# Kernel tuning notes

Measured on AMD Instinct MI355X. Metric: run time of the kernel, lower is better.

## Reference

```python
import jax, jax.numpy as jnp
import numpy as np

NUM_HEADS = 16

def _alibi(S, H, dtype):
    # fairseq-style ALiBi: slopes[h] * -(|i-j|), H assumed power of 2
    start = 2.0 ** (-8.0 / H)
    slopes = start ** jnp.arange(1, H + 1, dtype=jnp.float32)      # [H]
    pos = jnp.arange(S)
    rel = -jnp.abs(pos[None, :] - pos[:, None]).astype(jnp.float32)  # [S,S]
    return (slopes[:, None, None] * rel).astype(dtype)             # [H,S,S]

def setup_inputs() -> dict:
    key = jax.random.key(0)
    kx, km, kw1, kw2 = jax.random.split(key, 4)
    B, S, D = 2, 2048, 1024
    inputs = jax.random.normal(kx, (B, S, D), dtype=jnp.float32)
    mask = jax.random.bernoulli(km, 0.9, (B, S))
    mask = mask.at[:, 0].set(True)  # ensure each row has a valid key
    Wqkv = jax.random.normal(kw1, (3 * D, D), dtype=jnp.float32) * 0.02
    bqkv = jnp.zeros((3 * D,), dtype=jnp.float32)
    Wproj = jax.random.normal(kw2, (D, D), dtype=jnp.float32) * 0.02
    bproj = jnp.zeros((D,), dtype=jnp.float32)
    return {"inputs": inputs, "mask": mask, "Wqkv": Wqkv, "bqkv": bqkv,
            "Wproj": Wproj, "bproj": bproj}

def reference(inputs, mask, Wqkv, bqkv, Wproj, bproj):
    B, S, D = inputs.shape
    H = NUM_HEADS
    dh = D // H
    scale = D ** (-0.5)  # NOTE: original scales by full dim, not head dim
    qkv = inputs @ Wqkv.T + bqkv                       # [B,S,3D]
    qkv = qkv.reshape(B, S, H, 3 * dh).transpose(0, 2, 1, 3)  # [B,H,S,3dh]
    q, k, v = qkv[..., :dh], qkv[..., dh:2 * dh], qkv[..., 2 * dh:]
    attn = jnp.einsum('bhqd,bhkd->bhqk', q, k) * scale  # [B,H,S,S]
    attn = attn + _alibi(S, H, attn.dtype)[None]
    attn = jnp.where(mask[:, None, None, :], attn, jnp.finfo(attn.dtype).min)
    attn = jax.nn.softmax(attn, axis=-1)
    x = jnp.einsum('bhqk,bhkd->bhqd', attn, v)          # [B,H,S,dh]
    x = x.transpose(0, 2, 1, 3).reshape(B, S, D)
    return x @ Wproj.T + bproj
```

## Files before the change

kernel.cpp:

```cpp
#include <hip/hip_runtime.h>
#include <cstdint>
#include <cstddef>

#define B_  2
#define S_  2048
#define D_  1024
#define H_  16
#define DH_ 64
#define M_  (B_*S_)
#define N3_ (3*D_)
#define NT_ (S_/64)

typedef float f32x4 __attribute__((ext_vector_type(4)));
typedef short short8 __attribute__((ext_vector_type(8)));
typedef unsigned short u16x8 __attribute__((ext_vector_type(8)));
typedef unsigned short u16x4 __attribute__((ext_vector_type(4)));

__device__ __forceinline__ unsigned short f2bf(float x) {
    unsigned int u = __float_as_uint(x);
    unsigned int r = (u + 0x7FFFu + ((u >> 16) & 1u)) >> 16;
    return (unsigned short)r;
}

__device__ __forceinline__ float exp2_(float x) { return __builtin_amdgcn_exp2f(x); }

__device__ __forceinline__ unsigned int cvt_pk_bf16(float a, float b) {
    unsigned int r;
    asm volatile("v_cvt_pk_bf16_f32 %0, %1, %2" : "=v"(r) : "v"(a), "v"(b));
    return r;
}

__device__ __forceinline__ void gload16(const void* g, void* l) {
    __builtin_amdgcn_global_load_lds(
        (const __attribute__((address_space(1))) unsigned int*)g,
        (__attribute__((address_space(3))) unsigned int*)l,
        16, 0, 0);
}

__global__ void k_detect_mask(const unsigned char* __restrict__ mb, int* __restrict__ flag) {
    __shared__ int sBig, sM4, sM8;
    if (threadIdx.x == 0) { sBig = 0; sM4 = 0; sM8 = 0; }
    __syncthreads();
    int big = 0, m4 = 0, m8 = 0;
    for (int i = threadIdx.x; i < 4096; i += blockDim.x) {
        unsigned char v = mb[i];
        if (v > 1) big = 1;
        if (v && (i & 3)) m4 = 1;
        if (v && ((i & 7) == 4)) m8 = 1;
    }
    if (big) atomicOr(&sBig, 1);
    if (m4)  atomicOr(&sM4, 1);
    if (m8)  atomicOr(&sM8, 1);
    __syncthreads();
    if (threadIdx.x == 0) {
        int w;
        if (sBig)      w = 0;
        else if (sM4)  w = 1;
        else if (sM8)  w = 4;
        else           w = 8;
        *flag = w;
    }
}

__global__ void k_maskbits(const void* __restrict__ mask, const int* __restrict__ flag,
                           unsigned long long* __restrict__ bits) {
    int i = blockIdx.x * 64 + threadIdx.x;
    int w = *flag;
    bool on;
    if (w == 0)      on = ((const float*)mask)[i] != 0.0f;
    else if (w == 1) on = ((const unsigned char*)mask)[i] != 0;
    else if (w == 4) on = ((const int*)mask)[i] != 0;
    else             on = ((const long long*)mask)[i] != 0;
    unsigned long long bal = __ballot(on);
    if (threadIdx.x == 0) bits[blockIdx.x] = bal;
}

__global__ void k_f2bf(const float* __restrict__ in, unsigned short* __restrict__ out, int n) {
    int i = (blockIdx.x * blockDim.x + threadIdx.x) * 4;
    if (i >= n) return;
    float4 v = *reinterpret_cast<const float4*>(&in[i]);
    u16x4 o = { f2bf(v.x), f2bf(v.y), f2bf(v.z), f2bf(v.w) };
    *reinterpret_cast<u16x4*>(&out[i]) = o;
}

template <bool OUT_BF16>
__global__ __launch_bounds__(256) void k_gemm_bf16_nt(
    const unsigned short* __restrict__ A, const unsigned short* __restrict__ W,
    const float* __restrict__ bias, void* __restrict__ Cout,
    int M, int N, int K) {
    __shared__ __align__(16) unsigned short Al[128 * 64];
    __shared__ __align__(16) unsigned short Wl[128 * 64];

    const int tid  = threadIdx.x;
    const int lane = tid & 63;
    const int w    = tid >> 6;
    const int wr   = w >> 1, wc = w & 1;
    const int l16  = lane & 15, g = lane >> 4;
    const int m0 = blockIdx.y * 128, n0 = blockIdx.x * 128;

    f32x4 acc[4][4];
#pragma unroll
    for (int m = 0; m < 4; ++m)
#pragma unroll
        for (int n = 0; n < 4; ++n) acc[m][n] = (f32x4){0.f, 0.f, 0.f, 0.f};

    const int srow = tid >> 3, scol = (tid & 7) * 8;

    for (int k0 = 0; k0 < K; k0 += 64) {
        __syncthreads();
#pragma unroll
        for (int i = 0; i < 4; ++i) {
            const int c = i * 256 + tid;
            const int row = srow + i * 32;
            gload16(A + (size_t)(m0 + row) * K + k0 + scol, Al + c * 8);
            gload16(W + (size_t)(n0 + row) * K + k0 + scol, Wl + c * 8);
        }
        __syncthreads();

#pragma unroll
        for (int kk = 0; kk < 2; ++kk) {
            short8 a[4], b[4];
#pragma unroll
            for (int m = 0; m < 4; ++m)
                a[m] = *reinterpret_cast<const short8*>(
                    &Al[(size_t)(wr * 64 + m * 16 + l16) * 64 + kk * 32 + g * 8]);
#pragma unroll
            for (int n = 0; n < 4; ++n)
                b[n] = *reinterpret_cast<const short8*>(
                    &Wl[(size_t)(wc * 64 + n * 16 + l16) * 64 + kk * 32 + g * 8]);
#pragma unroll
            for (int m = 0; m < 4; ++m)
#pragma unroll
                for (int n = 0; n < 4; ++n)
                    acc[m][n] = __builtin_amdgcn_mfma_f32_16x16x32_bf16(a[m], b[n], acc[m][n], 0, 0, 0);
        }
    }

    float bv[4];
#pragma unroll
    for (int n = 0; n < 4; ++n) bv[n] = bias[n0 + wc * 64 + n * 16 + l16];
#pragma unroll
    for (int m = 0; m < 4; ++m) {
#pragma unroll
        for (int r = 0; r < 4; ++r) {
            const size_t row = m0 + wr * 64 + m * 16 + g * 4 + r;
#pragma unroll
            for (int n = 0; n < 4; ++n) {
                const int col = n0 + wc * 64 + n * 16 + l16;
                float v = acc[m][n][r] + bv[n];
                if (OUT_BF16)
                    ((unsigned short*)Cout)[row * N + col] = f2bf(v);
                else
                    ((float*)Cout)[row * N + col] = v;
            }
        }
    }
}

__global__ __launch_bounds__(256) void k_attn_mfma(
    const unsigned short* __restrict__ qkv,
    const unsigned long long* __restrict__ mbits,
    unsigned short* __restrict__ x) {
    __shared__ __align__(16) unsigned short Kt[64][72];
    __shared__ __align__(16) unsigned short Vt[64][72];
    __shared__ __align__(16) unsigned short QP[64][72];

    const int tid  = threadIdx.x;
    const int lane = tid & 63;
    const int wq   = tid >> 6;
    const int g    = lane >> 4;
    const int g4   = g * 4;
    const int l16  = lane & 15;

    const int nqt = S_ / 64;
    const int qt = blockIdx.x % nqt;
    const int h  = (blockIdx.x / nqt) % H_;
    const int b  = blockIdx.x / (nqt * H_);
    const int q0 = qt * 64;
    const size_t rowbase = (size_t)b * S_ * N3_;
    const int hq = h * 192, hk = hq + 64, hv = hq + 128;
    const unsigned short* kvb = qkv + rowbase;

    {
        const int row = tid >> 2, cb = (tid & 3) * 16;
        const unsigned short* src = kvb + (size_t)(q0 + row) * N3_ + hq + cb;
        *reinterpret_cast<u16x8*>(&QP[row][cb])     = *reinterpret_cast<const u16x8*>(src);
        *reinterpret_cast<u16x8*>(&QP[row][cb + 8]) = *reinterpret_cast<const u16x8*>(src + 8);
    }
    __syncthreads();

    const short8 qa0 = *reinterpret_cast<const short8*>(&QP[wq*16 + l16][g*8]);
    const short8 qa1 = *reinterpret_cast<const short8*>(&QP[wq*16 + l16][32 + g*8]);

    f32x4 Oacc[4];
#pragma unroll
    for (int df = 0; df < 4; ++df) Oacc[df] = (f32x4){0.f, 0.f, 0.f, 0.f};
    float m = -1e30f, l = 0.0f;

    const float LOG2E = 1.4426950408889634f;
    const float c1 = 0.03125f * LOG2E;
    const float c2 = exp2f(-0.5f * (float)(h + 1)) * LOG2E;
    const int   qg = q0 + wq * 16 + l16;
    float albr[4];
#pragma unroll
    for (int r = 0; r < 4; ++r) albr[r] = c2 * (float)(g4 + r);
    const float c2_16 = c2 * 16.0f;

    const int krow = tid >> 2, kcb = (tid & 3) * 16;
    const int vkb = (tid & 15) * 4, vdb = (tid >> 4) * 4;
    u16x8 kr0, kr1;
    u16x4 vr0, vr1, vr2, vr3;

    {
        const unsigned short* ks = kvb + (size_t)krow * N3_ + hk + kcb;
        kr0 = *reinterpret_cast<const u16x8*>(ks);
        kr1 = *reinterpret_cast<const u16x8*>(ks + 8);
        const unsigned short* vs = kvb + (size_t)vkb * N3_ + hv + vdb;
        vr0 = *reinterpret_cast<const u16x4*>(vs);
        vr1 = *reinterpret_cast<const u16x4*>(vs + N3_);
        vr2 = *reinterpret_cast<const u16x4*>(vs + 2 * N3_);
        vr3 = *reinterpret_cast<const u16x4*>(vs + 3 * N3_);
    }

    for (int t = 0; t < NT_; ++t) {
        const int k0 = t * 64;
        __syncthreads();

        *reinterpret_cast<u16x8*>(&Kt[krow][kcb])     = kr0;
        *reinterpret_cast<u16x8*>(&Kt[krow][kcb + 8]) = kr1;
        {
            u16x4 w0 = { vr0.x, vr1.x, vr2.x, vr3.x };
            u16x4 w1 = { vr0.y, vr1.y, vr2.y, vr3.y };
            u16x4 w2 = { vr0.z, vr1.z, vr2.z, vr3.z };
            u16x4 w3 = { vr0.w, vr1.w, vr2.w, vr3.w };
            *reinterpret_cast<u16x4*>(&Vt[vdb + 0][vkb]) = w0;
            *reinterpret_cast<u16x4*>(&Vt[vdb + 1][vkb]) = w1;
            *reinterpret_cast<u16x4*>(&Vt[vdb + 2][vkb]) = w2;
            *reinterpret_cast<u16x4*>(&Vt[vdb + 3][vkb]) = w3;
        }
        if (t + 1 < NT_) {
            const int kn = k0 + 64;
            const unsigned short* ks = kvb + (size_t)(kn + krow) * N3_ + hk + kcb;
            kr0 = *reinterpret_cast<const u16x8*>(ks);
            kr1 = *reinterpret_cast<const u16x8*>(ks + 8);
            const unsigned short* vs = kvb + (size_t)(kn + vkb) * N3_ + hv + vdb;
            vr0 = *reinterpret_cast<const u16x4*>(vs);
            vr1 = *reinterpret_cast<const u16x4*>(vs + N3_);
            vr2 = *reinterpret_cast<const u16x4*>(vs + 2 * N3_);
            vr3 = *reinterpret_cast<const u16x4*>(vs + 3 * N3_);
        }
        __syncthreads();

        float p_[4][4];
#pragma unroll
        for (int jb = 0; jb < 4; ++jb) {
            short8 kb0 = *reinterpret_cast<const short8*>(&Kt[jb*16 + l16][g*8]);
            short8 kb1 = *reinterpret_cast<const short8*>(&Kt[jb*16 + l16][32 + g*8]);
            f32x4 c = (f32x4){0.f, 0.f, 0.f, 0.f};
            c = __builtin_amdgcn_mfma_f32_16x16x32_bf16(kb0, qa0, c, 0, 0, 0);
            c = __builtin_amdgcn_mfma_f32_16x16x32_bf16(kb1, qa1, c, 0, 0, 0);
#pragma unroll
            for (int r = 0; r < 4; ++r) p_[jb][r] = c[r];
        }

        if (k0 < q0) {
            const float tb = c2 * (float)(k0 - qg);
#pragma unroll
            for (int jb = 0; jb < 4; ++jb) {
                const float tbj = tb + c2_16 * (float)jb;
#pragma unroll
                for (int r = 0; r < 4; ++r)
                    p_[jb][r] = fmaf(p_[jb][r], c1, tbj + albr[r]);
            }
        } else if (k0 > q0) {
            const float tb = c2 * (float)(k0 - qg);
#pragma unroll
            for (int jb = 0; jb < 4; ++jb) {
                const float tbj = -tb - c2_16 * (float)jb;
#pragma unroll
                for (int r = 0; r < 4; ++r)
                    p_[jb][r] = fmaf(p_[jb][r], c1, tbj - albr[r]);
            }
        } else {
            const int dbase = k0 - qg;
#pragma unroll
            for (int jb = 0; jb < 4; ++jb)
#pragma unroll
                for (int r = 0; r < 4; ++r) {
                    int d = dbase + jb * 16 + g4 + r;
                    d = d < 0 ? -d : d;
                    p_[jb][r] = fmaf(p_[jb][r], c1, -c2 * (float)d);
                }
        }

        float mx = p_[0][0];
#pragma unroll
        for (int jb = 0; jb < 4; ++jb)
#pragma unroll
            for (int r = 0; r < 4; ++r) mx = fmaxf(mx, p_[jb][r]);
        mx = fmaxf(mx, __shfl_xor(mx, 16));
        mx = fmaxf(mx, __shfl_xor(mx, 32));

        if (__any(mx > m + 8.0f)) {
            const float mn = fmaxf(m, mx);
            const float cr = exp2_(m - mn);
            m = mn;
            l *= cr;
            const int srcb = (lane & 48) + ((lane & 48) >> 2);
#pragma unroll
            for (int r = 0; r < 4; ++r) {
                const float crq = __shfl(cr, srcb + r);
#pragma unroll
                for (int df = 0; df < 4; ++df) Oacc[df][r] *= crq;
            }
        }

        const unsigned long long mb = mbits[b * NT_ + t];
        const unsigned long long msh = mb >> g4;
        const unsigned int mw0 = (unsigned int)msh;
        const unsigned int mw1 = (unsigned int)(msh >> 32);
        float ps = 0.0f;
#pragma unroll
        for (int jb = 0; jb < 4; ++jb)
#pragma unroll
            for (int r = 0; r < 4; ++r) {
                float p = exp2_(p_[jb][r] - m);
                const unsigned int w = (jb < 2) ? mw0 : mw1;
                const int idx = (jb & 1) * 16 + r;
                p = ((w >> idx) & 1u) ? p : 0.0f;
                p_[jb][r] = p;
                ps += p;
            }
        ps += __shfl_xor(ps, 16);
        ps += __shfl_xor(ps, 32);
        l += ps;

#pragma unroll
        for (int jb = 0; jb < 4; ++jb) {
            uint2 st;
            st.x = cvt_pk_bf16(p_[jb][0], p_[jb][1]);
            st.y = cvt_pk_bf16(p_[jb][2], p_[jb][3]);
            *reinterpret_cast<uint2*>(&QP[wq*16 + l16][jb*16 + g4]) = st;
        }

        const short8 pa0 = *reinterpret_cast<const short8*>(&QP[wq*16 + l16][g*8]);
        const short8 pa1 = *reinterpret_cast<const short8*>(&QP[wq*16 + l16][32 + g*8]);
#pragma unroll
        for (int df = 0; df < 4; ++df) {
            short8 vb0 = *reinterpret_cast<const short8*>(&Vt[df*16 + l16][g*8]);
            short8 vb1 = *reinterpret_cast<const short8*>(&Vt[df*16 + l16][32 + g*8]);
            Oacc[df] = __builtin_amdgcn_mfma_f32_16x16x32_bf16(pa0, vb0, Oacc[df], 0, 0, 0);
            Oacc[df] = __builtin_amdgcn_mfma_f32_16x16x32_bf16(pa1, vb1, Oacc[df], 0, 0, 0);
        }
    }

    const int srcb = (lane & 48) + ((lane & 48) >> 2);
    float invq[4];
#pragma unroll
    for (int r = 0; r < 4; ++r) invq[r] = 1.0f / __shfl(l, srcb + r);
#pragma unroll
    for (int df = 0; df < 4; ++df) {
#pragma unroll
        for (int r = 0; r < 4; ++r) {
            const int qrow = q0 + wq * 16 + g4 + r;
            x[(size_t)(b * S_ + qrow) * D_ + h * 64 + df * 16 + l16] = f2bf(Oacc[df][r] * invq[r]);
        }
    }
}

extern "C" void kernel_launch(void* const* d_in, const int* in_sizes, int n_in,
                              void* d_out, int out_size, void* d_ws, size_t ws_size,
                              hipStream_t stream) {
    const float* inputs = (const float*)d_in[0];
    const void*  mask   = d_in[1];
    const float* Wqkv   = (const float*)d_in[2];
    const float* bqkv   = (const float*)d_in[3];
    const float* Wproj  = (const float*)d_in[4];
    const float* bproj  = (const float*)d_in[5];
    float* out = (float*)d_out;

    unsigned short* qkvb = (unsigned short*)d_ws;
    unsigned short* xb   = qkvb + (size_t)M_ * N3_;
    unsigned short* Ab   = xb + (size_t)M_ * D_;
    unsigned short* Wqb  = Ab + (size_t)M_ * D_;
    unsigned short* Wpb  = Wqb + (size_t)N3_ * D_;
    unsigned long long* bits = (unsigned long long*)(Wpb + (size_t)D_ * D_);
    int* flag = (int*)(bits + B_ * NT_);

    k_detect_mask<<<1, 256, 0, stream>>>((const unsigned char*)mask, flag);
    k_maskbits<<<B_ * NT_, 64, 0, stream>>>(mask, flag, bits);

    k_f2bf<<<(M_ * D_ / 4 + 255) / 256, 256, 0, stream>>>(inputs, Ab, M_ * D_);
    k_f2bf<<<(N3_ * D_ / 4 + 255) / 256, 256, 0, stream>>>(Wqkv, Wqb, N3_ * D_);
    k_f2bf<<<(D_ * D_ / 4 + 255) / 256, 256, 0, stream>>>(Wproj, Wpb, D_ * D_);

    dim3 g1(N3_ / 128, M_ / 128);
    k_gemm_bf16_nt<true><<<g1, 256, 0, stream>>>(Ab, Wqb, bqkv, qkvb, M_, N3_, D_);

    k_attn_mfma<<<B_ * H_ * (S_ / 64), 256, 0, stream>>>(qkvb, bits, xb);

    dim3 g2(D_ / 128, M_ / 128);
    k_gemm_bf16_nt<false><<<g2, 256, 0, stream>>>(xb, Wpb, bproj, out, M_, D_, D_);
}
```

Baseline: 194.2 us.

## Precompute additive mask in LDS, add MFMA priority hints, defer row-sum reduction

Expands the per-batch key mask bits into an additive float bias array in shared memory once per block and folds it into the score FMA. This removes the per-element bit tests and select from the softmax loop. It also wraps both MFMA phases in s_setprio to favour matrix issue across waves, rebalances the max reduction into a tree, and moves the row-sum shuffles after the PV MFMAs to overlap them. The cost is an extra 8KB of LDS per block, which may reduce occupancy, and a -1e30 bias whose correctness relies on exp2 underflowing to zero.

```diff
diff --git a/kernel.cpp b/kernel.cpp
--- a/kernel.cpp
+++ b/kernel.cpp
@@ -164,6 +164,7 @@
     __shared__ __align__(16) unsigned short Kt[64][72];
     __shared__ __align__(16) unsigned short Vt[64][72];
     __shared__ __align__(16) unsigned short QP[64][72];
+    __shared__ __align__(16) float Am[S_];
 
     const int tid  = threadIdx.x;
     const int lane = tid & 63;
@@ -180,6 +181,15 @@
     const size_t rowbase = (size_t)b * S_ * N3_;
     const int hq = h * 192, hk = hq + 64, hv = hq + 128;
     const unsigned short* kvb = qkv + rowbase;
+
+    {
+#pragma unroll
+        for (int it = 0; it < S_ / 256; ++it) {
+            const int k = it * 256 + tid;
+            const unsigned long long w = mbits[b * NT_ + (k >> 6)];
+            Am[k] = ((w >> (k & 63)) & 1ull) ? 0.0f : -1e30f;
+        }
+    }
 
     {
         const int row = tid >> 2, cb = (tid & 3) * 16;
@@ -252,6 +262,7 @@
         __syncthreads();
 
         float p_[4][4];
+        __builtin_amdgcn_s_setprio(1);
 #pragma unroll
         for (int jb = 0; jb < 4; ++jb) {
             short8 kb0 = *reinterpret_cast<const short8*>(&Kt[jb*16 + l16][g*8]);
@@ -262,6 +273,12 @@
 #pragma unroll
             for (int r = 0; r < 4; ++r) p_[jb][r] = c[r];
         }
+        __builtin_amdgcn_s_setprio(0);
+
+        f32x4 amv[4];
+#pragma unroll
+        for (int jb = 0; jb < 4; ++jb)
+            amv[jb] = *reinterpret_cast<const f32x4*>(&Am[k0 + jb * 16 + g4]);
 
         if (k0 < q0) {
             const float tb = c2 * (float)(k0 - qg);
@@ -270,7 +287,7 @@
                 const float tbj = tb + c2_16 * (float)jb;
 #pragma unroll
                 for (int r = 0; r < 4; ++r)
-                    p_[jb][r] = fmaf(p_[jb][r], c1, tbj + albr[r]);
+                    p_[jb][r] = fmaf(p_[jb][r], c1, tbj + albr[r] + amv[jb][r]);
             }
         } else if (k0 > q0) {
             const float tb = c2 * (float)(k0 - qg);
@@ -279,7 +296,7 @@
                 const float tbj = -tb - c2_16 * (float)jb;
 #pragma unroll
                 for (int r = 0; r < 4; ++r)
-                    p_[jb][r] = fmaf(p_[jb][r], c1, tbj - albr[r]);
+                    p_[jb][r] = fmaf(p_[jb][r], c1, tbj - albr[r] + amv[jb][r]);
             }
         } else {
             const int dbase = k0 - qg;
@@ -289,15 +306,18 @@
                 for (int r = 0; r < 4; ++r) {
                     int d = dbase + jb * 16 + g4 + r;
                     d = d < 0 ? -d : d;
-                    p_[jb][r] = fmaf(p_[jb][r], c1, -c2 * (float)d);
+                    p_[jb][r] = fmaf(p_[jb][r], c1, amv[jb][r] - c2 * (float)d);
                 }
         }
 
-        float mx = p_[0][0];
-#pragma unroll
-        for (int jb = 0; jb < 4; ++jb)
-#pragma unroll
-            for (int r = 0; r < 4; ++r) mx = fmaxf(mx, p_[jb][r]);
+        float mx;
+        {
+            float m0_ = fmaxf(fmaxf(p_[0][0], p_[0][1]), fmaxf(p_[0][2], p_[0][3]));
+            float m1_ = fmaxf(fmaxf(p_[1][0], p_[1][1]), fmaxf(p_[1][2], p_[1][3]));
+            float m2_ = fmaxf(fmaxf(p_[2][0], p_[2][1]), fmaxf(p_[2][2], p_[2][3]));
+            float m3_ = fmaxf(fmaxf(p_[3][0], p_[3][1]), fmaxf(p_[3][2], p_[3][3]));
+            mx = fmaxf(fmaxf(m0_, m1_), fmaxf(m2_, m3_));
+        }
         mx = fmaxf(mx, __shfl_xor(mx, 16));
         mx = fmaxf(mx, __shfl_xor(mx, 32));
 
@@ -315,25 +335,15 @@
             }
         }
 
-        const unsigned long long mb = mbits[b * NT_ + t];
-        const unsigned long long msh = mb >> g4;
-        const unsigned int mw0 = (unsigned int)msh;
-        const unsigned int mw1 = (unsigned int)(msh >> 32);
         float ps = 0.0f;
 #pragma unroll
         for (int jb = 0; jb < 4; ++jb)
 #pragma unroll
             for (int r = 0; r < 4; ++r) {
                 float p = exp2_(p_[jb][r] - m);
-                const unsigned int w = (jb < 2) ? mw0 : mw1;
-                const int idx = (jb & 1) * 16 + r;
-                p = ((w >> idx) & 1u) ? p : 0.0f;
                 p_[jb][r] = p;
                 ps += p;
             }
-        ps += __shfl_xor(ps, 16);
-        ps += __shfl_xor(ps, 32);
-        l += ps;
 
 #pragma unroll
         for (int jb = 0; jb < 4; ++jb) {
@@ -345,6 +355,7 @@
 
         const short8 pa0 = *reinterpret_cast<const short8*>(&QP[wq*16 + l16][g*8]);
         const short8 pa1 = *reinterpret_cast<const short8*>(&QP[wq*16 + l16][32 + g*8]);
+        __builtin_amdgcn_s_setprio(1);
 #pragma unroll
         for (int df = 0; df < 4; ++df) {
             short8 vb0 = *reinterpret_cast<const short8*>(&Vt[df*16 + l16][g*8]);
@@ -352,6 +363,11 @@
             Oacc[df] = __builtin_amdgcn_mfma_f32_16x16x32_bf16(pa0, vb0, Oacc[df], 0, 0, 0);
             Oacc[df] = __builtin_amdgcn_mfma_f32_16x16x32_bf16(pa1, vb1, Oacc[df], 0, 0, 0);
         }
+        __builtin_amdgcn_s_setprio(0);
+
+        ps += __shfl_xor(ps, 16);
+        ps += __shfl_xor(ps, 32);
+        l += ps;
     }
 
     const int srcb = (lane & 48) + ((lane & 48) >> 2);
```

Measured after the change: 200.4 us. +3.2%, slower.
